# Kernel tuning notes

Measured on AMD Instinct MI355X. Metric: run time of the kernel, lower is better.

The kernel has to match this reference:

```python
import jax, jax.numpy as jnp
import numpy as np


def _register_translation(target_images, src_images, upsample_factor):
    # squeeze channel dim -> (B, H, W), promote to complex for FFT
    tgt = target_images[..., 0].astype(jnp.complex64)
    src = src_images[..., 0].astype(jnp.complex64)
    B, H, W = tgt.shape

    target_freq = jnp.fft.fft2(tgt)
    src_freq = jnp.fft.fft2(src)
    # cross-power spectrum (skimage register_translation convention)
    image_product = src_freq * jnp.conj(target_freq)
    cross_corr = jnp.fft.ifft2(image_product)

    # coarse (integer-pixel) peak
    abs_cc = jnp.abs(cross_corr).reshape(B, -1)
    idx = jnp.argmax(abs_cc, axis=1)
    maxima = jnp.stack([idx // W, idx % W], axis=1).astype(jnp.float32)  # (B,2)
    shape_f = jnp.array([H, W], jnp.float32)
    midpoints = jnp.array([H // 2, W // 2], jnp.float32)  # fix(axis_size/2)
    shifts = jnp.where(maxima > midpoints, maxima - shape_f, maxima)

    if upsample_factor > 1:
        uf = float(upsample_factor)
        shifts = jnp.round(shifts * uf) / uf
        region = int(np.ceil(upsample_factor * 1.5))  # upsampled region size
        dftshift = float(np.fix(region / 2.0))
        offsets = dftshift - shifts * uf  # (B,2) sample region offsets

        r_idx = jnp.arange(region, dtype=jnp.float32)
        freq_r = (jnp.fft.fftfreq(H) * H).astype(jnp.float32)  # ifftshift(arange(H)-H//2)
        freq_c = (jnp.fft.fftfreq(W) * W).astype(jnp.float32)
        two_pi = 2.0 * np.pi

        # per-batch small DFT kernels: row (B, region, H), col (B, W, region)
        row_ang = (two_pi / (H * uf)) * (r_idx[None, :, None] - offsets[:, 0][:, None, None]) * freq_r[None, None, :]
        col_ang = (two_pi / (W * uf)) * freq_c[None, :, None] * (r_idx[None, None, :] - offsets[:, 1][:, None, None])
        row_k = jnp.exp(-1j * row_ang)
        col_k = jnp.exp(-1j * col_ang)

        # upsampled DFT of conj(image_product), then conjugate back
        cc_up = jnp.conj(jnp.einsum('brh,bhw,bwc->brc', row_k, jnp.conj(image_product), col_k))
        abs_up = jnp.abs(cc_up).reshape(B, -1)
        idx2 = jnp.argmax(abs_up, axis=1)
        max2 = jnp.stack([idx2 // region, idx2 % region], axis=1).astype(jnp.float32) - dftshift
        shifts = shifts + max2 / uf

    return shifts  # (B, 2) -- (row_shift, col_shift)


def setup_inputs() -> dict:
    key = jax.random.key(0)
    k1, k2 = jax.random.split(key)
    B, H, W = 32, 512, 512
    target_images = jax.random.normal(k1, (B, H, W, 1), dtype=jnp.float32)
    src_images = jax.random.normal(k2, (B, H, W, 1), dtype=jnp.float32)
    return {"target_images": target_images, "src_images": src_images, "upsample_factor": 20}


def reference(target_images, src_images, upsample_factor):
    return _register_translation(target_images, src_images, upsample_factor)
```

## Files before the change

kernel.cpp:

```cpp
#include <hip/hip_runtime.h>
#include <math.h>

#define BN 32
#define HN 512
#define WN 512
#define REGION 30
#define RPAD 32
#define UFV 20.0f
#define DFTSHIFT 15.0f
#define TWO_PI 6.2831853071795864769f
#define HS 8
#define HCH (HN / HS)
#define WS 4

typedef float2 cplx;

__device__ __forceinline__ cplx cmul(cplx a, cplx b){
    return make_float2(a.x*b.x - a.y*b.y, a.x*b.y + a.y*b.x);
}
__device__ __forceinline__ cplx cadd(cplx a, cplx b){
    return make_float2(a.x + b.x, a.y + b.y);
}
__device__ __forceinline__ cplx csub(cplx a, cplx b){
    return make_float2(a.x - b.x, a.y - b.y);
}
__device__ __forceinline__ int brev9(int i){ return (int)(__brev((unsigned)i) >> 23); }
__device__ __forceinline__ int brev6(int i){ return (int)(__brev((unsigned)i) >> 26); }
__device__ __forceinline__ int csl(int h, int c){ return c * 546 + h + (h >> 4); }

#define BFLY(a,b,w){ cplx t_ = cmul(w,b); b = make_float2(a.x - t_.x, a.y - t_.y); a = cadd(a, t_); }
#define BFLY1(a,b){ cplx t_ = b; b = make_float2(a.x - t_.x, a.y - t_.y); a = cadd(a, t_); }

__device__ __forceinline__ void fft512_regs(cplx* v, const float2* tw, cplx* ds, int lane){
    const cplx wI  = *(const cplx*)&tw[128];
    const cplx w8a = *(const cplx*)&tw[64];
    const cplx w8b = *(const cplx*)&tw[192];
    BFLY1(v[0],v[1]); BFLY1(v[2],v[3]); BFLY1(v[4],v[5]); BFLY1(v[6],v[7]);
    BFLY1(v[0],v[2]); BFLY(v[1],v[3],wI); BFLY1(v[4],v[6]); BFLY(v[5],v[7],wI);
    BFLY1(v[0],v[4]); BFLY(v[1],v[5],w8a); BFLY(v[2],v[6],wI); BFLY(v[3],v[7],w8b);
    const int h = lane >> 3, lo = lane & 7;
    const int bw = 9 * lane;
    const int br = 72 * h + lo;
    #pragma unroll
    for (int j = 0; j < 8; ++j) ds[bw + j] = v[j];
    asm volatile("s_waitcnt lgkmcnt(0)" ::: "memory");
    #pragma unroll
    for (int j = 0; j < 8; ++j) v[j] = ds[br + 9*j];
    {
        cplx wA = *(const cplx*)&tw[lo<<5];
        BFLY(v[0],v[1],wA); BFLY(v[2],v[3],wA); BFLY(v[4],v[5],wA); BFLY(v[6],v[7],wA);
        cplx wB0 = *(const cplx*)&tw[lo<<4], wB1 = *(const cplx*)&tw[128+(lo<<4)];
        BFLY(v[0],v[2],wB0); BFLY(v[1],v[3],wB1); BFLY(v[4],v[6],wB0); BFLY(v[5],v[7],wB1);
        cplx wC0 = *(const cplx*)&tw[lo<<3], wC1 = *(const cplx*)&tw[64+(lo<<3)];
        cplx wC2 = *(const cplx*)&tw[128+(lo<<3)], wC3 = *(const cplx*)&tw[192+(lo<<3)];
        BFLY(v[0],v[4],wC0); BFLY(v[1],v[5],wC1); BFLY(v[2],v[6],wC2); BFLY(v[3],v[7],wC3);
    }
    #pragma unroll
    for (int j = 0; j < 8; ++j) ds[br + 9*j] = v[j];
    asm volatile("s_waitcnt lgkmcnt(0)" ::: "memory");
    const int br3 = lane + (lane >> 3);
    #pragma unroll
    for (int j = 0; j < 8; ++j) v[j] = ds[br3 + 72*j];
    {
        cplx wD = *(const cplx*)&tw[lane<<2];
        BFLY(v[0],v[1],wD); BFLY(v[2],v[3],wD); BFLY(v[4],v[5],wD); BFLY(v[6],v[7],wD);
        cplx wE0 = *(const cplx*)&tw[lane<<1], wE1 = *(const cplx*)&tw[128+(lane<<1)];
        BFLY(v[0],v[2],wE0); BFLY(v[1],v[3],wE1); BFLY(v[4],v[6],wE0); BFLY(v[5],v[7],wE1);
        cplx wF0 = *(const cplx*)&tw[lane], wF1 = *(const cplx*)&tw[64+lane];
        cplx wF2 = *(const cplx*)&tw[128+lane], wF3 = *(const cplx*)&tw[192+lane];
        BFLY(v[0],v[4],wF0); BFLY(v[1],v[5],wF1); BFLY(v[2],v[6],wF2); BFLY(v[3],v[7],wF3);
    }
}

__global__ void __launch_bounds__(256) row_fft_pack(const float* __restrict__ tgt,
                                                    const float* __restrict__ src,
                                                    cplx* __restrict__ Fz){
    __shared__ float2 tw[256];
    __shared__ cplx ds[4 * 576];
    const int tid = threadIdx.x;
    { float sv, cv; sincosf(-TWO_PI * (float)tid * (1.0f/512.0f), &sv, &cv);
      tw[tid] = make_float2(cv, sv); }
    __syncthreads();
    const int wave = tid >> 6, lane = tid & 63;
    const int rid = blockIdx.x * 4 + wave;
    const float* tr = tgt + (size_t)rid * WN;
    const float* sr = src + (size_t)rid * WN;
    const int rb6 = brev6(lane);
    const int B3[8] = {0,256,128,384,64,320,192,448};
    cplx v[8];
    #pragma unroll
    for (int j = 0; j < 8; ++j){ int o = B3[j] + rb6; v[j] = make_float2(tr[o], sr[o]); }
    fft512_regs(v, (const float2*)tw, ds + wave * 576, lane);
    cplx* orow = Fz + (size_t)rid * WN;
    #pragma unroll
    for (int j = 0; j < 8; ++j) orow[64*j + lane] = v[j];
}

__device__ __forceinline__ void col_fft8_t512(cplx* sm, const float2* tw, int tid){
    const cplx wI  = tw[128];
    const cplx w8a = tw[64];
    const cplx w8b = tw[192];
    const int c = tid & 7;
    const int k = tid >> 3;
    {
        cplx y[8];
        #pragma unroll
        for (int m = 0; m < 8; ++m) y[m] = sm[csl(8*k + m, c)];
        BFLY1(y[0],y[1]); BFLY1(y[2],y[3]); BFLY1(y[4],y[5]); BFLY1(y[6],y[7]);
        BFLY1(y[0],y[2]); BFLY(y[1],y[3],wI); BFLY1(y[4],y[6]); BFLY(y[5],y[7],wI);
        BFLY1(y[0],y[4]); BFLY(y[1],y[5],w8a); BFLY(y[2],y[6],wI); BFLY(y[3],y[7],w8b);
        #pragma unroll
        for (int m = 0; m < 8; ++m) sm[csl(8*k + m, c)] = y[m];
    }
    __syncthreads();
    #pragma unroll
    for (int pass = 1; pass < 3; ++pass){
        const int st = 3*pass + 1;
        const int h1 = 1 << (st - 1);
        const int q = k & (h1 - 1);
        const int i0 = ((k >> (st - 1)) << (st + 2)) + q;
        cplx x[8];
        #pragma unroll
        for (int m = 0; m < 8; ++m) x[m] = sm[csl(i0 + m*h1, c)];
        cplx w1 = tw[q << (9 - st)];
        BFLY(x[0],x[1],w1); BFLY(x[2],x[3],w1); BFLY(x[4],x[5],w1); BFLY(x[6],x[7],w1);
        cplx w2a = tw[q << (8 - st)];
        cplx w2b = tw[(q << (8 - st)) + 128];
        BFLY(x[0],x[2],w2a); BFLY(x[1],x[3],w2b); BFLY(x[4],x[6],w2a); BFLY(x[5],x[7],w2b);
        cplx w30 = tw[q << (7 - st)];
        cplx w31 = tw[(q << (7 - st)) + 64];
        cplx w32 = tw[(q << (7 - st)) + 128];
        cplx w33 = tw[(q << (7 - st)) + 192];
        BFLY(x[0],x[4],w30); BFLY(x[1],x[5],w31); BFLY(x[2],x[6],w32); BFLY(x[3],x[7],w33);
        #pragma unroll
        for (int m = 0; m < 8; ++m) sm[csl(i0 + m*h1, c)] = x[m];
        __syncthreads();
    }
}

__global__ void __launch_bounds__(512) col_fft_fwd(cplx* __restrict__ buf){
    const int b  = blockIdx.y;
    const int w0 = blockIdx.x * 8;
    const int tid = threadIdx.x;
    __shared__ cplx sm[4368];
    __shared__ float2 tw[256];
    if (tid < 256){ float sv, cv; sincosf(-TWO_PI * (float)tid * (1.0f/512.0f), &sv, &cv);
      tw[tid] = make_float2(cv, sv); }
    cplx* base = buf + (size_t)b * HN * WN + w0;
    for (int idx = tid; idx < HN * 4; idx += 512){
        int h = idx >> 2, c2 = (idx & 3) << 1;
        float4 v = *(const float4*)(base + (size_t)h * WN + c2);
        int hb = brev9(h);
        sm[csl(hb, c2)]     = make_float2(v.x, v.y);
        sm[csl(hb, c2 + 1)] = make_float2(v.z, v.w);
    }
    __syncthreads();
    col_fft8_t512(sm, (const float2*)tw, tid);
    for (int idx = tid; idx < HN * 4; idx += 512){
        int h = idx >> 2, c2 = (idx & 3) << 1;
        cplx a = sm[csl(h, c2)], d = sm[csl(h, c2 + 1)];
        *(float4*)(base + (size_t)h * WN + c2) = make_float4(a.x, a.y, d.x, d.y);
    }
}

__global__ void __launch_bounds__(256) cross_rowinv(cplx* __restrict__ Fz, cplx* __restrict__ cc){
    __shared__ float2 tw[256];
    __shared__ cplx ds[4 * 1184];
    const int tid = threadIdx.x;
    { float sv, cv; sincosf(TWO_PI * (float)tid * (1.0f/512.0f), &sv, &cv);
      tw[tid] = make_float2(cv, sv); }
    __syncthreads();
    const int wave = tid >> 6, lane = tid & 63;
    const int p = blockIdx.x * 4 + wave;
    if (p > 256) return;
    const int b = blockIdx.y;
    const int h1 = p, h2 = (HN - p) & (HN - 1);
    cplx* r1 = Fz + ((size_t)b * HN + h1) * WN;
    cplx* r2 = Fz + ((size_t)b * HN + h2) * WN;
    cplx* A = ds + wave * 1184;
    cplx* B = A + 592;
    #pragma unroll
    for (int u = 0; u < 8; ++u){
        A[lane + 64*u] = r1[lane + 64*u];
        B[lane + 64*u] = r2[lane + 64*u];
    }
    asm volatile("s_waitcnt lgkmcnt(0)" ::: "memory");
    const int rb6 = brev6(lane);
    const int B3[8] = {0,256,128,384,64,320,192,448};
    cplx v1[8];
    #pragma unroll
    for (int j = 0; j < 8; ++j){
        int w  = B3[j] + rb6;
        int wm = (WN - w) & (WN - 1);
        cplx Aw = A[w], Bw = B[w], Am = A[wm], Bm = B[wm];
        { cplx Bc = make_float2(Bm.x, -Bm.y);
          cplx s = cadd(Aw, Bc);
          cplx d = make_float2(Aw.x - Bc.x, Aw.y - Bc.y);
          cplx D = make_float2(d.x*s.x + d.y*s.y, d.y*s.x - d.x*s.y);
          v1[j] = make_float2(0.25f * D.y, -0.25f * D.x); }
        if (w < 320){
          cplx Ac = make_float2(Am.x, -Am.y);
          cplx s = cadd(Bw, Ac);
          cplx d = make_float2(Bw.x - Ac.x, Bw.y - Ac.y);
          cplx D = make_float2(d.x*s.x + d.y*s.y, d.y*s.x - d.x*s.y);
          r2[w] = make_float2(0.25f * D.y, -0.25f * D.x);
          r1[w] = v1[j];
        }
    }
    fft512_regs(v1, (const float2*)tw, A, lane);
    cplx* c1 = cc + ((size_t)b * HN + h1) * WN;
    #pragma unroll
    for (int j = 0; j < 8; ++j) c1[64*j + lane] = v1[j];
}

__global__ void __launch_bounds__(512) colinv_argmax(const cplx* __restrict__ buf,
                                                     float2* __restrict__ cand){
    const int b  = blockIdx.y;
    const int w0 = blockIdx.x * 8;
    const int tid = threadIdx.x;
    __shared__ cplx sm[4368];
    __shared__ float2 tw[256];
    __shared__ float wv_[8];
    __shared__ int   wi_[8];
    if (tid < 256){ float sv, cv; sincosf(TWO_PI * (float)tid * (1.0f/512.0f), &sv, &cv);
      tw[tid] = make_float2(cv, sv); }
    const cplx* base = buf + (size_t)b * HN * WN + w0;
    for (int idx = tid; idx < 257 * 4; idx += 512){
        int h = idx >> 2, c2 = (idx & 3) << 1;
        float4 v = *(const float4*)(base + (size_t)h * WN + c2);
        int hb = brev9(h);
        sm[csl(hb, c2)]     = make_float2(v.x, v.y);
        sm[csl(hb, c2 + 1)] = make_float2(v.z, v.w);
    }
    __syncthreads();
    for (int idx = tid; idx < 255 * 8; idx += 512){
        int h = 257 + (idx >> 3), c = idx & 7;
        cplx v = sm[csl(brev9(HN - h), c)];
        sm[csl(brev9(h), c)] = make_float2(v.x, -v.y);
    }
    __syncthreads();
    col_fft8_t512(sm, (const float2*)tw, tid);
    float best = -1.0f; int bidx = 0x7fffffff;
    for (int idx = tid; idx < HN * 8; idx += 512){
        int h = idx >> 3, c = idx & 7;
        cplx v = sm[csl(h, c)];
        float mm = v.x * v.x + v.y * v.y;
        if (mm > best){ best = mm; bidx = h * WN + w0 + c; }
    }
    for (int off = 32; off > 0; off >>= 1){
        float v2 = __shfl_down(best, off);
        int   i2 = __shfl_down(bidx, off);
        if (v2 > best || (v2 == best && i2 < bidx)){ best = v2; bidx = i2; }
    }
    if ((tid & 63) == 0){ wv_[tid >> 6] = best; wi_[tid >> 6] = bidx; }
    __syncthreads();
    if (tid == 0){
        float bv = wv_[0]; int bx = wi_[0];
        #pragma unroll
        for (int w2 = 1; w2 < 8; ++w2){
            if (wv_[w2] > bv || (wv_[w2] == bv && wi_[w2] < bx)){ bv = wv_[w2]; bx = wi_[w2]; }
        }
        cand[b * 64 + blockIdx.x] = make_float2(bv, __int_as_float(bx));
    }
}

__global__ void coarse_reduce(const float2* __restrict__ cand, float* __restrict__ small){
    const int b = blockIdx.x, t = threadIdx.x;
    float2 c = cand[b * 64 + t];
    float v = c.x; int ix = __float_as_int(c.y);
    for (int off = 32; off > 0; off >>= 1){
        float v2 = __shfl_down(v, off);
        int   i2 = __shfl_down(ix, off);
        if (v2 > v || (v2 == v && i2 < ix)){ v = v2; ix = i2; }
    }
    if (t == 0){
        int row = ix / WN, col = ix % WN;
        float sr = (row > HN / 2) ? (float)(row - HN) : (float)row;
        float sc = (col > WN / 2) ? (float)(col - WN) : (float)col;
        small[b * 4 + 0] = sr;
        small[b * 4 + 1] = sc;
        small[b * 4 + 2] = DFTSHIFT - sr * UFV;
        small[b * 4 + 3] = DFTSHIFT - sc * UFV;
    }
}

__global__ void __launch_bounds__(256, 3) upsample_T(const cplx* __restrict__ P,
                                                     const float* __restrict__ small,
                                                     cplx* __restrict__ Tpart){
    const int b = blockIdx.y, hs = blockIdx.z;
    const int tid = threadIdx.x;
    const int wp = tid & 31;
    const int rbase = tid >> 5;
    const int w = blockIdx.x * 64 + wp * 2;
    const int h0 = hs * HCH;
    const float off0 = small[b * 4 + 2];
    const float CC = TWO_PI / (HN * UFV);
    __shared__ float2 rk[RPAD][HCH];
    for (int idx = tid; idx < RPAD * HCH; idx += 256){
        int r = idx >> 6, hh = idx & (HCH - 1);
        int h = h0 + hh;
        float fr = (h < HN / 2) ? (float)h : (float)(h - HN);
        float sv, cv; sincosf(-CC * ((float)r - off0) * fr, &sv, &cv);
        rk[r][hh] = make_float2(cv, sv);
    }
    __syncthreads();
    cplx a0[4], a1[4];
    #pragma unroll
    for (int u = 0; u < 4; ++u){ a0[u] = make_float2(0.f,0.f); a1[u] = make_float2(0.f,0.f); }
    const cplx* pc = P + ((size_t)b * HN + h0) * WN + w;

    float4 pvA[4], pvB[4];
    #pragma unroll
    for (int k = 0; k < 4; ++k) pvA[k] = *(const float4*)(pc + (size_t)k * WN);

    #pragma unroll 1
    for (int hh = 0; hh < HCH; hh += 8){
        #pragma unroll
        for (int k = 0; k < 4; ++k)
            pvB[k] = *(const float4*)(pc + (size_t)(hh + 4 + k) * WN);
        #pragma unroll
        for (int k = 0; k < 4; ++k){
            #pragma unroll
            for (int u = 0; u < 4; ++u){
                cplx wv = rk[rbase * 4 + u][hh + k];
                a0[u].x += wv.x * pvA[k].x + wv.y * pvA[k].y;
                a0[u].y += wv.y * pvA[k].x - wv.x * pvA[k].y;
                a1[u].x += wv.x * pvA[k].z + wv.y * pvA[k].w;
                a1[u].y += wv.y * pvA[k].z - wv.x * pvA[k].w;
            }
        }
        if (hh + 8 < HCH){
            #pragma unroll
            for (int k = 0; k < 4; ++k)
                pvA[k] = *(const float4*)(pc + (size_t)(hh + 8 + k) * WN);
        }
        #pragma unroll
        for (int k = 0; k < 4; ++k){
            #pragma unroll
            for (int u = 0; u < 4; ++u){
                cplx wv = rk[rbase * 4 + u][hh + 4 + k];
                a0[u].x += wv.x * pvB[k].x + wv.y * pvB[k].y;
                a0[u].y += wv.y * pvB[k].x - wv.x * pvB[k].y;
                a1[u].x += wv.x * pvB[k].z + wv.y * pvB[k].w;
                a1[u].y += wv.y * pvB[k].z - wv.x * pvB[k].w;
            }
        }
    }

    #pragma unroll
    for (int u = 0; u < 4; ++u){
        int r = rbase * 4 + u;
        if (r < REGION){
            float4* dst = (float4*)(Tpart + (((size_t)hs * BN + b) * REGION + r) * WN + w);
            *dst = make_float4(a0[u].x, a0[u].y, a1[u].x, a1[u].y);
        }
    }
}

__global__ void upsample_U_part(const cplx* __restrict__ Tpart, const cplx* __restrict__ P,
                                const float* __restrict__ small, cplx* __restrict__ Upart){
    const int ws = blockIdx.x, b = blockIdx.y;
    const int tid = threadIdx.x;
    const int w0 = ws * 64;
    const float off0 = small[b * 4 + 2];
    const float off1 = small[b * 4 + 3];
    const float CW = TWO_PI / (WN * UFV);
    const float CH = TWO_PI / (HN * UFV);
    __shared__ float2 Ts[REGION][64];
    __shared__ float2 ck[64][REGION];
    __shared__ float2 p256[64];
    __shared__ float2 T256s[REGION];
    const size_t TS = (size_t)BN * REGION * WN;
    for (int idx = tid; idx < REGION * 64; idx += 256){
        int r = idx >> 6, ww = idx & 63;
        cplx s = make_float2(0.f, 0.f);
        #pragma unroll
        for (int hs = 0; hs < HS; ++hs)
            s = cadd(s, Tpart[(size_t)hs * TS + ((size_t)b * REGION + r) * WN + w0 + ww]);
        Ts[r][ww] = s;
    }
    if (tid < 64) p256[tid] = P[((size_t)b * HN + 256) * WN + w0 + tid];
    if (ws == 0 && tid >= 64 && tid < 64 + REGION){
        int r = tid - 64;
        cplx s = make_float2(0.f, 0.f);
        #pragma unroll
        for (int hs = 0; hs < HS; ++hs)
            s = cadd(s, Tpart[(size_t)hs * TS + ((size_t)b * REGION + r) * WN + 256]);
        T256s[r] = s;
    }
    for (int idx = tid; idx < 64 * REGION; idx += 256){
        int ww = idx / REGION, c = idx - ww * REGION;
        int w = w0 + ww;
        float sv, cv; sincosf(-CW * (float)w * ((float)c - off1), &sv, &cv);
        ck[ww][c] = make_float2(cv, sv);
    }
    __syncthreads();
    const int start = (ws == 0) ? 1 : 0;
    #pragma unroll
    for (int q = 0; q < 4; ++q){
        int o = tid + 256 * q;
        if (o < REGION * REGION){
            int r = o / REGION, c = o - r * REGION;
            float racc = 0.f;
            cplx s2 = make_float2(0.f, 0.f);
            for (int ww = start; ww < 64; ++ww){
                float2 T = Ts[r][ww], K = ck[ww][c];
                racc += T.x * K.x - T.y * K.y;
                float2 pv = p256[ww];
                s2.x += pv.x * K.x + pv.y * K.y;
                s2.y += pv.y * K.x - pv.x * K.y;
            }
            float th = CH * ((float)r - off0) * 256.0f;
            float snt = sinf(th);
            cplx contrib = make_float2(2.f * racc - 2.f * snt * s2.y,
                                       2.f * snt * s2.x);
            if (ws == 0){
                contrib = cadd(contrib, Ts[r][0]);
                float s256, c256; sincosf(CW * 256.0f * ((float)c - off1), &s256, &c256);
                contrib = cadd(contrib, cmul(T256s[r], make_float2(c256, s256)));
            }
            Upart[((size_t)ws * BN + b) * (REGION * REGION) + o] = contrib;
        }
    }
}

__global__ void upsample_argmax(const cplx* __restrict__ Upart, const float* __restrict__ small,
                                float* __restrict__ out){
    const int b = blockIdx.x;
    const int tid = threadIdx.x;
    float best = -1.0f; int bidx = 0x7fffffff;
    #pragma unroll
    for (int q = 0; q < 4; ++q){
        int o = tid + 256 * q;
        if (o < REGION * REGION){
            cplx u = make_float2(0.f, 0.f);
            #pragma unroll
            for (int ws = 0; ws < WS; ++ws)
                u = cadd(u, Upart[((size_t)ws * BN + b) * (REGION * REGION) + o]);
            float m = u.x * u.x + u.y * u.y;
            if (m > best){ best = m; bidx = o; }
        }
    }
    __shared__ float vals[256];
    __shared__ int   idxs[256];
    vals[tid] = best; idxs[tid] = bidx;
    __syncthreads();
    for (int s = 128; s > 0; s >>= 1){
        if (tid < s){
            if (vals[tid + s] > vals[tid] ||
                (vals[tid + s] == vals[tid] && idxs[tid + s] < idxs[tid])){
                vals[tid] = vals[tid + s]; idxs[tid] = idxs[tid + s];
            }
        }
        __syncthreads();
    }
    if (tid == 0){
        int o = idxs[0];
        float r = (float)(o / REGION) - DFTSHIFT;
        float c = (float)(o % REGION) - DFTSHIFT;
        out[b * 2 + 0] = small[b * 4 + 0] + r / UFV;
        out[b * 2 + 1] = small[b * 4 + 1] + c / UFV;
    }
}

extern "C" void kernel_launch(void* const* d_in, const int* in_sizes, int n_in,
                              void* d_out, int out_size, void* d_ws, size_t ws_size,
                              hipStream_t stream){
    const float* tgt = (const float*)d_in[0];
    const float* src = (const float*)d_in[1];
    float* out = (float*)d_out;

    const size_t BIG = (size_t)BN * HN * WN;
    cplx* buf1 = (cplx*)d_ws;
    cplx* buf2 = buf1 + BIG;
    float* small = (float*)(buf2 + BIG);
    float2* cand = (float2*)(small + 128);

    const size_t TSTRIDE = (size_t)BN * REGION * WN;
    cplx* Tpart = buf2;
    cplx* Upart = buf2 + HS * TSTRIDE;

    dim3 blk(256);
    row_fft_pack<<<dim3(BN * HN / 4), blk, 0, stream>>>(tgt, src, buf1);
    col_fft_fwd<<<dim3(WN / 8, BN), dim3(512), 0, stream>>>(buf1);
    cross_rowinv<<<dim3((257 + 3) / 4, BN), blk, 0, stream>>>(buf1, buf2);
    colinv_argmax<<<dim3(WN / 8, BN), dim3(512), 0, stream>>>(buf2, cand);
    coarse_reduce<<<dim3(BN), dim3(64), 0, stream>>>(cand, small);
    upsample_T<<<dim3(5, BN, HS), blk, 0, stream>>>(buf1, small, Tpart);
    upsample_U_part<<<dim3(WS, BN), blk, 0, stream>>>(Tpart, buf1, small, Upart);
    upsample_argmax<<<dim3(BN), blk, 0, stream>>>(Upart, small, out);
}
```

Measured before the change: 177.6 us.

## Transpose row-DFT shared table and compute column 256 separately in U kernel

The row-kernel table in upsample_T is transposed so each thread fetches its four twiddles with two vector shared loads instead of four strided ones. The fifth block column of upsample_T, which existed only to produce column 256, is dropped. upsample_U_part now computes that column's row-DFT directly from P using in-kernel sincos and a small shuffle reduction. This trims a partially used block per batch and cuts LDS traffic, at the cost of extra serial work in the ws==0 blocks.

```diff
diff --git a/kernel.cpp b/kernel.cpp
--- a/kernel.cpp
+++ b/kernel.cpp
@@ -295,13 +295,13 @@
     const int h0 = hs * HCH;
     const float off0 = small[b * 4 + 2];
     const float CC = TWO_PI / (HN * UFV);
-    __shared__ float2 rk[RPAD][HCH];
-    for (int idx = tid; idx < RPAD * HCH; idx += 256){
-        int r = idx >> 6, hh = idx & (HCH - 1);
+    __shared__ float2 rkT[HCH][RPAD];
+    for (int idx = tid; idx < HCH * RPAD; idx += 256){
+        int hh = idx >> 5, r = idx & 31;
         int h = h0 + hh;
         float fr = (h < HN / 2) ? (float)h : (float)(h - HN);
         float sv, cv; sincosf(-CC * ((float)r - off0) * fr, &sv, &cv);
-        rk[r][hh] = make_float2(cv, sv);
+        rkT[hh][r] = make_float2(cv, sv);
     }
     __syncthreads();
     cplx a0[4], a1[4];
@@ -320,13 +320,16 @@
             pvB[k] = *(const float4*)(pc + (size_t)(hh + 4 + k) * WN);
         #pragma unroll
         for (int k = 0; k < 4; ++k){
+            float4 rk01 = *(const float4*)&rkT[hh + k][rbase * 4];
+            float4 rk23 = *(const float4*)&rkT[hh + k][rbase * 4 + 2];
+            float wvx[4] = {rk01.x, rk01.z, rk23.x, rk23.z};
+            float wvy[4] = {rk01.y, rk01.w, rk23.y, rk23.w};
             #pragma unroll
             for (int u = 0; u < 4; ++u){
-                cplx wv = rk[rbase * 4 + u][hh + k];
-                a0[u].x += wv.x * pvA[k].x + wv.y * pvA[k].y;
-                a0[u].y += wv.y * pvA[k].x - wv.x * pvA[k].y;
-                a1[u].x += wv.x * pvA[k].z + wv.y * pvA[k].w;
-                a1[u].y += wv.y * pvA[k].z - wv.x * pvA[k].w;
+                a0[u].x += wvx[u] * pvA[k].x + wvy[u] * pvA[k].y;
+                a0[u].y += wvy[u] * pvA[k].x - wvx[u] * pvA[k].y;
+                a1[u].x += wvx[u] * pvA[k].z + wvy[u] * pvA[k].w;
+                a1[u].y += wvy[u] * pvA[k].z - wvx[u] * pvA[k].w;
             }
         }
         if (hh + 8 < HCH){
@@ -336,13 +339,16 @@
         }
         #pragma unroll
         for (int k = 0; k < 4; ++k){
+            float4 rk01 = *(const float4*)&rkT[hh + 4 + k][rbase * 4];
+            float4 rk23 = *(const float4*)&rkT[hh + 4 + k][rbase * 4 + 2];
+            float wvx[4] = {rk01.x, rk01.z, rk23.x, rk23.z};
+            float wvy[4] = {rk01.y, rk01.w, rk23.y, rk23.w};
             #pragma unroll
             for (int u = 0; u < 4; ++u){
-                cplx wv = rk[rbase * 4 + u][hh + 4 + k];
-                a0[u].x += wv.x * pvB[k].x + wv.y * pvB[k].y;
-                a0[u].y += wv.y * pvB[k].x - wv.x * pvB[k].y;
-                a1[u].x += wv.x * pvB[k].z + wv.y * pvB[k].w;
-                a1[u].y += wv.y * pvB[k].z - wv.x * pvB[k].w;
+                a0[u].x += wvx[u] * pvB[k].x + wvy[u] * pvB[k].y;
+                a0[u].y += wvy[u] * pvB[k].x - wvx[u] * pvB[k].y;
+                a1[u].x += wvx[u] * pvB[k].z + wvy[u] * pvB[k].w;
+                a1[u].y += wvy[u] * pvB[k].z - wvx[u] * pvB[k].w;
             }
         }
     }
@@ -370,6 +376,7 @@
     __shared__ float2 ck[64][REGION];
     __shared__ float2 p256[64];
     __shared__ float2 T256s[REGION];
+    __shared__ float2 pcol[HN];
     const size_t TS = (size_t)BN * REGION * WN;
     for (int idx = tid; idx < REGION * 64; idx += 256){
         int r = idx >> 6, ww = idx & 63;
@@ -380,13 +387,9 @@
         Ts[r][ww] = s;
     }
     if (tid < 64) p256[tid] = P[((size_t)b * HN + 256) * WN + w0 + tid];
-    if (ws == 0 && tid >= 64 && tid < 64 + REGION){
-        int r = tid - 64;
-        cplx s = make_float2(0.f, 0.f);
-        #pragma unroll
-        for (int hs = 0; hs < HS; ++hs)
-            s = cadd(s, Tpart[(size_t)hs * TS + ((size_t)b * REGION + r) * WN + 256]);
-        T256s[r] = s;
+    if (ws == 0){
+        for (int h = tid; h < HN; h += 256)
+            pcol[h] = P[((size_t)b * HN + h) * WN + 256];
     }
     for (int idx = tid; idx < 64 * REGION; idx += 256){
         int ww = idx / REGION, c = idx - ww * REGION;
@@ -395,6 +398,28 @@
         ck[ww][c] = make_float2(cv, sv);
     }
     __syncthreads();
+    if (ws == 0){
+        int idx = tid - 64;
+        if (idx >= 0 && idx < REGION * 8){
+            int r = idx >> 3, ch = idx & 7;
+            float rr = (float)r - off0;
+            cplx s = make_float2(0.f, 0.f);
+            for (int h = ch * 64; h < ch * 64 + 64; ++h){
+                float fr = (h < HN / 2) ? (float)h : (float)(h - HN);
+                float sv, cv; sincosf(-CH * rr * fr, &sv, &cv);
+                float2 p = pcol[h];
+                s.x += cv * p.x + sv * p.y;
+                s.y += sv * p.x - cv * p.y;
+            }
+            #pragma unroll
+            for (int off = 4; off > 0; off >>= 1){
+                s.x += __shfl_down(s.x, off, 8);
+                s.y += __shfl_down(s.y, off, 8);
+            }
+            if (ch == 0) T256s[r] = s;
+        }
+        __syncthreads();
+    }
     const int start = (ws == 0) ? 1 : 0;
     #pragma unroll
     for (int q = 0; q < 4; ++q){
@@ -486,7 +511,7 @@
     cross_rowinv<<<dim3((257 + 3) / 4, BN), blk, 0, stream>>>(buf1, buf2);
     colinv_argmax<<<dim3(WN / 8, BN), dim3(512), 0, stream>>>(buf2, cand);
     coarse_reduce<<<dim3(BN), dim3(64), 0, stream>>>(cand, small);
-    upsample_T<<<dim3(5, BN, HS), blk, 0, stream>>>(buf1, small, Tpart);
+    upsample_T<<<dim3(4, BN, HS), blk, 0, stream>>>(buf1, small, Tpart);
     upsample_U_part<<<dim3(WS, BN), blk, 0, stream>>>(Tpart, buf1, small, Upart);
     upsample_argmax<<<dim3(BN), blk, 0, stream>>>(Upart, small, out);
 }
```

After: 181.1 us. No clear change (+2.0%).
